# Kernel tuning notes

Measured on AMD Instinct MI355X. Metric: run time of the kernel, lower is better.

The kernel has to match this reference:

```python
import jax, jax.numpy as jnp
import numpy as np

BATCH, SEQ, DMODEL, DHID = 4, 4096, 1024, 1024
R_MIN, R_MAX = 0.9, 0.99
MAX_PHASE = np.pi / 50  # module overrides ctor arg with pi/50
EPS = 1e-5


def setup_inputs() -> dict:
    key = jax.random.key(0)
    ks = jax.random.split(key, 8)
    # nu_init
    u1 = jax.random.uniform(ks[0], (DHID,)) * (1 - EPS) + EPS
    mag_sq = u1 * (R_MAX ** 2 - R_MIN ** 2) + R_MIN ** 2
    nu_log = jnp.log(-0.5 * jnp.log(mag_sq + EPS))
    # theta_init
    u2 = jax.random.uniform(ks[1], (DHID,)) * (1 - EPS) + EPS
    theta_log = jnp.log(MAX_PHASE * u2)
    B_re = jax.random.normal(ks[2], (DHID, DMODEL)) / np.sqrt(2 * DMODEL)
    B_im = jax.random.normal(ks[3], (DHID, DMODEL)) / np.sqrt(2 * DMODEL)
    C_re = jax.random.normal(ks[4], (DMODEL, DHID)) / np.sqrt(DHID)
    C_im = jax.random.normal(ks[5], (DMODEL, DHID)) / np.sqrt(DHID)
    D_skip = jax.random.normal(ks[6], (DMODEL,))
    inputs = jax.random.normal(ks[7], (BATCH, SEQ, DMODEL), dtype=jnp.float32)
    return {"inputs": inputs, "nu_log": nu_log, "theta_log": theta_log,
            "B_re": B_re, "B_im": B_im, "C_re": C_re, "C_im": C_im,
            "D_skip": D_skip}


def reference(inputs, nu_log, theta_log, B_re, B_im, C_re, C_im, D_skip):
    nu = jnp.exp(nu_log)
    theta = jnp.exp(theta_log)
    diag_lambda = jnp.exp(-nu + 1j * theta)            # [H] complex
    # forward recomputes gamma_log from nu_log (parameter gamma_log unused)
    gamma_log = 0.5 * jnp.log(1 - jnp.exp(-2 * jnp.exp(nu_log)) + EPS)
    B_norm = (B_re + 1j * B_im) * jnp.exp(gamma_log)[:, None]  # [H, D]
    inputs_c = inputs.astype(jnp.complex64)
    Bu = jnp.einsum('hd,btd->bth', B_norm, inputs_c)   # [B, T, H]

    def step(h, bu_t):
        h = diag_lambda * h + bu_t
        return h, h

    h0 = jnp.zeros((inputs.shape[0], diag_lambda.shape[0]), dtype=Bu.dtype)
    _, hs = jax.lax.scan(step, h0, jnp.swapaxes(Bu, 0, 1))  # [T, B, H]
    hs = jnp.swapaxes(hs, 0, 1)                              # [B, T, H]
    C_complex = C_re + 1j * C_im                              # [D, H]
    out = jnp.einsum('bth,dh->btd', hs, C_complex).real + inputs * D_skip
    return out.astype(jnp.float32)
```

## Files before the change

kernel.cpp:

```cpp
#include <hip/hip_runtime.h>


typedef __bf16 bf16x8 __attribute__((ext_vector_type(8)));
typedef float floatx4 __attribute__((ext_vector_type(4)));

__device__ __forceinline__ unsigned short f2bf(float f) {
  unsigned u = __float_as_uint(f);
  u += 0x7fffu + ((u >> 16) & 1u);
  return (unsigned short)(u >> 16);
}
__device__ __forceinline__ float bf2f(unsigned short s) {
  return __uint_as_float(((unsigned)s) << 16);
}


__global__ void prep_params(const float* __restrict__ nu_log,
                            const float* __restrict__ theta_log,
                            float* __restrict__ lam,
                            float* __restrict__ lamL,
                            float* __restrict__ gamma)
{
  int h = blockIdx.x * 256 + threadIdx.x;
  float nu = expf(nu_log[h]);
  float th = expf(theta_log[h]);
  float r = expf(-nu);
  lam[h]        = r * cosf(th);
  lam[1024 + h] = r * sinf(th);
  float rL = expf(-128.0f * nu);
  lamL[h]        = rL * cosf(128.0f * th);
  lamL[1024 + h] = rL * sinf(128.0f * th);
  gamma[h] = sqrtf(1.0f - expf(-2.0f * nu) + 1e-5f);
}

__global__ void prep_B(const float* __restrict__ B_re, const float* __restrict__ B_im,
                       const float* __restrict__ gamma, unsigned short* __restrict__ Bcat)
{
  int tid = blockIdx.x * 256 + threadIdx.x;
  int n = tid >> 10;
  int d = tid & 1023;
  int h = n & 1023;
  float v = (n < 1024 ? B_re[h * 1024 + d] : B_im[h * 1024 + d]) * gamma[h];
  Bcat[tid] = f2bf(v);
}

__global__ void prep_C(const float* __restrict__ C_re, const float* __restrict__ C_im,
                       unsigned short* __restrict__ Ccat)
{
  int tid = blockIdx.x * 256 + threadIdx.x;
  int d = tid >> 11;
  int k = tid & 2047;
  float v = (k < 1024) ? C_re[d * 1024 + k] : -C_im[d * 1024 + (k - 1024)];
  Ccat[tid] = f2bf(v);
}

__global__ void conv_inputs(const float* __restrict__ in, unsigned short* __restrict__ outb)
{
  int tid = blockIdx.x * 256 + threadIdx.x;
  float4 v = ((const float4*)in)[tid];
  unsigned lo = (unsigned)f2bf(v.x) | ((unsigned)f2bf(v.y) << 16);
  unsigned hi = (unsigned)f2bf(v.z) | ((unsigned)f2bf(v.w) << 16);
  ((uint2*)outb)[tid] = make_uint2(lo, hi);
}


#define GLDS(gp, lp) __builtin_amdgcn_global_load_lds(                        \
      (const __attribute__((address_space(1))) void*)(gp),                    \
      (__attribute__((address_space(3))) void*)(lp), 16, 0, 0)

#define STAGE(kt, buf) do {                                                   \
    const int _ko = (kt) * 32;                                                \
    GLDS(gA0 + _ko, &As[(buf)][lofs0]);                                       \
    GLDS(gA1 + _ko, &As[(buf)][lofs1]);                                       \
    GLDS(gB0 + _ko, &Bs[(buf)][lofs0]);                                       \
    GLDS(gB1 + _ko, &Bs[(buf)][lofs1]);                                       \
  } while (0)

#define BODY(buf) do {                                                        \
    bf16x8 af[8], bf[4];                                                      \
    _Pragma("unroll")                                                         \
    for (int i = 0; i < 8; ++i) {                                             \
      const int r = wm * 128 + i * 16 + lm;                                   \
      af[i] = *reinterpret_cast<const bf16x8*>(                               \
          &As[(buf)][r * 32 + (q ^ ((r >> 1) & 3)) * 8]);                     \
    }                                                                         \
    _Pragma("unroll")                                                         \
    for (int j = 0; j < 4; ++j) {                                             \
      const int r = wn * 64 + j * 16 + lm;                                    \
      bf[j] = *reinterpret_cast<const bf16x8*>(                               \
          &Bs[(buf)][r * 32 + (q ^ ((r >> 1) & 3)) * 8]);                     \
    }                                                                         \
    __builtin_amdgcn_s_setprio(1);                                            \
    _Pragma("unroll")                                                         \
    for (int i = 0; i < 8; ++i)                                               \
      _Pragma("unroll")                                                       \
      for (int j = 0; j < 4; ++j)                                             \
        acc[i][j] = __builtin_amdgcn_mfma_f32_16x16x32_bf16(                  \
            af[i], bf[j], acc[i][j], 0, 0, 0);                                \
    __builtin_amdgcn_s_setprio(0);                                            \
  } while (0)

#define RING_SYNC(vm) do {                                                    \
    __builtin_amdgcn_sched_barrier(0);                                        \
    asm volatile("s_waitcnt vmcnt(" #vm ")" ::: "memory");                    \
    __builtin_amdgcn_s_barrier();                                             \
    asm volatile("" ::: "memory");                                            \
  } while (0)

template <int EPI>
__global__ __launch_bounds__(512, 2) void gemm256_kernel(
    const unsigned short* __restrict__ A,
    const unsigned short* __restrict__ Bt,
    void* __restrict__ Cout,
    int M, int N, int K,
    const float* __restrict__ skip_in,
    const float* __restrict__ skip_w)
{
  __shared__ __align__(16) unsigned short As[4][256 * 32];
  __shared__ __align__(16) unsigned short Bs[4][256 * 32];

  const int tid  = threadIdx.x;
  const int lane = tid & 63;
  const int wave = tid >> 6;
  const int wm = wave >> 2;
  const int wn = wave & 3;

  const int flat    = blockIdx.x;
  const int xcd     = flat & 7;
  const int local   = flat >> 3;
  const int m_tile  = xcd * 8 + (local & 7);
  const int n_tile  = local >> 3;
  const int m0 = m_tile * 256;
  const int n0 = n_tile * 256;

  const int ldr = lane >> 2;
  const int pos = lane & 3;
  const int lm  = lane & 15;
  const int q   = lane >> 4;

  const int r0 = wave * 32 + ldr;
  const int r1 = r0 + 16;
  const int ca0 = pos ^ ((r0 >> 1) & 3);
  const int ca1 = pos ^ ((r1 >> 1) & 3);

  const unsigned short* gA0 = A  + (size_t)(m0 + r0) * K + ca0 * 8;
  const unsigned short* gA1 = A  + (size_t)(m0 + r1) * K + ca1 * 8;
  const unsigned short* gB0 = Bt + (size_t)(n0 + r0) * K + ca0 * 8;
  const unsigned short* gB1 = Bt + (size_t)(n0 + r1) * K + ca1 * 8;
  const int lofs0 = r0 * 32 + pos * 8;
  const int lofs1 = r1 * 32 + pos * 8;

  floatx4 acc[8][4];
#pragma unroll
  for (int i = 0; i < 8; ++i)
#pragma unroll
    for (int j = 0; j < 4; ++j)
      acc[i][j] = (floatx4){0.f, 0.f, 0.f, 0.f};

  const int KT = K >> 5;

  STAGE(0, 0);
  STAGE(1, 1);
  STAGE(2, 2);
  asm volatile("s_waitcnt vmcnt(8)" ::: "memory");
  __builtin_amdgcn_s_barrier();
  asm volatile("" ::: "memory");

  for (int kt = 0; kt + 3 < KT; ++kt) {
    STAGE(kt + 3, (kt + 3) & 3);
    BODY(kt & 3);
    RING_SYNC(8);
  }
  BODY((KT - 3) & 3);
  RING_SYNC(4);
  BODY((KT - 2) & 3);
  RING_SYNC(0);
  BODY((KT - 1) & 3);

#pragma unroll
  for (int i = 0; i < 8; ++i) {
#pragma unroll
    for (int j = 0; j < 4; ++j) {
      const int row0 = m0 + wm * 128 + i * 16 + q * 4;
      const int col  = n0 + wn * 64 + j * 16 + lm;
#pragma unroll
      for (int r = 0; r < 4; ++r) {
        const size_t idx = (size_t)(row0 + r) * N + col;
        if (EPI == 0) {
          ((unsigned short*)Cout)[idx] = f2bf(acc[i][j][r]);
        } else {
          ((float*)Cout)[idx] = acc[i][j][r] + skip_in[idx] * skip_w[col];
        }
      }
    }
  }
}


__global__ void scan_finals(const unsigned short* __restrict__ Bu,
                            const float* __restrict__ lam,
                            float2* __restrict__ finals)
{
  int tid = blockIdx.x * 256 + threadIdx.x;
  int h = tid & 1023, c = (tid >> 10) & 31, b = tid >> 15;
  float lre = lam[h], lim = lam[1024 + h];
  const unsigned short* p = Bu + ((size_t)(b * 4096 + c * 128) * 2048) + h;
  float yre = 0.f, yim = 0.f;
#pragma unroll 4
  for (int t = 0; t < 128; ++t) {
    float ure = bf2f(p[0]);
    float uim = bf2f(p[1024]);
    float nre = fmaf(lre, yre, fmaf(-lim, yim, ure));
    float nim = fmaf(lre, yim, fmaf(lim, yre, uim));
    yre = nre; yim = nim;
    p += 2048;
  }
  finals[tid] = make_float2(yre, yim);
}

__global__ void scan_carries(const float2* __restrict__ finals,
                             const float* __restrict__ lamL,
                             float2* __restrict__ carry)
{
  int tid = blockIdx.x * 256 + threadIdx.x;
  int h = tid & 1023, b = tid >> 10;
  float Lre = lamL[h], Lim = lamL[1024 + h];
  float Hre = 0.f, Him = 0.f;
  for (int c = 0; c < 32; ++c) {
    size_t i = ((size_t)(b * 32 + c) << 10) + h;
    carry[i] = make_float2(Hre, Him);
    float2 f = finals[i];
    float nre = fmaf(Lre, Hre, fmaf(-Lim, Him, f.x));
    float nim = fmaf(Lre, Him, fmaf(Lim, Hre, f.y));
    Hre = nre; Him = nim;
  }
}

__global__ void scan_apply(const float* __restrict__ lam,
                           const float2* __restrict__ carry,
                           unsigned short* __restrict__ Bu)
{
  int tid = blockIdx.x * 256 + threadIdx.x;
  int h = tid & 1023, c = (tid >> 10) & 31, b = tid >> 15;
  float lre = lam[h], lim = lam[1024 + h];
  float2 cv = carry[tid];
  float yre = cv.x, yim = cv.y;
  unsigned short* p = Bu + ((size_t)(b * 4096 + c * 128) * 2048) + h;
#pragma unroll 4
  for (int t = 0; t < 128; ++t) {
    float ure = bf2f(p[0]);
    float uim = bf2f(p[1024]);
    float nre = fmaf(lre, yre, fmaf(-lim, yim, ure));
    float nim = fmaf(lre, yim, fmaf(lim, yre, uim));
    yre = nre; yim = nim;
    p[0]    = f2bf(yre);
    p[1024] = f2bf(yim);
    p += 2048;
  }
}


extern "C" void kernel_launch(void* const* d_in, const int* in_sizes, int n_in,
                              void* d_out, int out_size, void* d_ws, size_t ws_size,
                              hipStream_t stream)
{
  const float* inputs    = (const float*)d_in[0];
  const float* nu_log    = (const float*)d_in[1];
  const float* theta_log = (const float*)d_in[2];
  const float* B_re      = (const float*)d_in[3];
  const float* B_im      = (const float*)d_in[4];
  const float* C_re      = (const float*)d_in[5];
  const float* C_im      = (const float*)d_in[6];
  const float* D_skip    = (const float*)d_in[7];
  float* out = (float*)d_out;

  char* ws = (char*)d_ws;
  float* lam   = (float*)ws;
  float* lamL  = lam + 2048;
  float* gamma = lamL + 2048;
  unsigned short* inp_bf = (unsigned short*)(ws + (1 << 16));
  unsigned short* Bcat   = inp_bf + (size_t)16384 * 1024;
  unsigned short* Ccat   = Bcat   + (size_t)2048 * 1024;
  unsigned short* Bu     = Ccat   + (size_t)1024 * 2048;
  float2* finals = (float2*)(Bu + (size_t)16384 * 2048);
  float2* carry  = finals + 131072;

  prep_params<<<4,    256, 0, stream>>>(nu_log, theta_log, lam, lamL, gamma);
  prep_B     <<<8192, 256, 0, stream>>>(B_re, B_im, gamma, Bcat);
  prep_C     <<<8192, 256, 0, stream>>>(C_re, C_im, Ccat);
  conv_inputs<<<16384,256, 0, stream>>>(inputs, inp_bf);

  gemm256_kernel<0><<<512, 512, 0, stream>>>(
      inp_bf, Bcat, Bu, 16384, 2048, 1024, nullptr, nullptr);

  scan_finals <<<512, 256, 0, stream>>>(Bu, lam, finals);
  scan_carries<<<16,  256, 0, stream>>>(finals, lamL, carry);
  scan_apply  <<<512, 256, 0, stream>>>(lam, carry, Bu);

  gemm256_kernel<1><<<256, 512, 0, stream>>>(
      Bu, Ccat, out, 16384, 1024, 2048, inputs, D_skip);
}
```

Baseline: 363.0 us.

## Split GEMM k-step into two barrier-separated phases interleaving LDS reads, loads, MFMAs

Each k-iteration of the 256x256 bf16 GEMM now runs as two half-phases. Each phase reads half of the A fragments from LDS, issues half of the next tile's global-to-LDS loads, and does 16 MFMAs between workgroup barriers, in a ping-pong style. The aim is to overlap LDS reads and global loads with matrix math across the waves and to cut register pressure by holding only 4 A fragments at a time. In exchange it doubles the number of barriers per k-step, and the hand-placed vmcnt waits and sched barriers depend on exact ordering.

```diff
diff --git a/kernel.cpp b/kernel.cpp
--- a/kernel.cpp
+++ b/kernel.cpp
@@ -75,35 +75,41 @@
     GLDS(gB1 + _ko, &Bs[(buf)][lofs1]);                                       \
   } while (0)
 
-#define BODY(buf) do {                                                        \
-    bf16x8 af[8], bf[4];                                                      \
-    _Pragma("unroll")                                                         \
-    for (int i = 0; i < 8; ++i) {                                             \
-      const int r = wm * 128 + i * 16 + lm;                                   \
-      af[i] = *reinterpret_cast<const bf16x8*>(                               \
-          &As[(buf)][r * 32 + (q ^ ((r >> 1) & 3)) * 8]);                     \
-    }                                                                         \
+#define READ_B(buf) do {                                                      \
     _Pragma("unroll")                                                         \
     for (int j = 0; j < 4; ++j) {                                             \
       const int r = wn * 64 + j * 16 + lm;                                    \
-      bf[j] = *reinterpret_cast<const bf16x8*>(                               \
+      bfr[j] = *reinterpret_cast<const bf16x8*>(                              \
           &Bs[(buf)][r * 32 + (q ^ ((r >> 1) & 3)) * 8]);                     \
     }                                                                         \
+  } while (0)
+
+#define READ_A(buf, i0) do {                                                  \
+    _Pragma("unroll")                                                         \
+    for (int i = 0; i < 4; ++i) {                                             \
+      const int r = wm * 128 + ((i0) + i) * 16 + lm;                          \
+      afr[i] = *reinterpret_cast<const bf16x8*>(                              \
+          &As[(buf)][r * 32 + (q ^ ((r >> 1) & 3)) * 8]);                     \
+    }                                                                         \
+  } while (0)
+
+#define MFMA16(i0) do {                                                       \
     __builtin_amdgcn_s_setprio(1);                                            \
     _Pragma("unroll")                                                         \
-    for (int i = 0; i < 8; ++i)                                               \
+    for (int i = 0; i < 4; ++i)                                               \
       _Pragma("unroll")                                                       \
       for (int j = 0; j < 4; ++j)                                             \
-        acc[i][j] = __builtin_amdgcn_mfma_f32_16x16x32_bf16(                  \
-            af[i], bf[j], acc[i][j], 0, 0, 0);                                \
+        acc[(i0) + i][j] = __builtin_amdgcn_mfma_f32_16x16x32_bf16(           \
+            afr[i], bfr[j], acc[(i0) + i][j], 0, 0, 0);                       \
     __builtin_amdgcn_s_setprio(0);                                            \
   } while (0)
 
-#define RING_SYNC(vm) do {                                                    \
+#define BAR() do {                                                            \
     __builtin_amdgcn_sched_barrier(0);                                        \
-    asm volatile("s_waitcnt vmcnt(" #vm ")" ::: "memory");                    \
+    asm volatile("" ::: "memory");                                            \
     __builtin_amdgcn_s_barrier();                                             \
     asm volatile("" ::: "memory");                                            \
+    __builtin_amdgcn_sched_barrier(0);                                        \
   } while (0)
 
 template <int EPI>
@@ -166,15 +172,65 @@
   asm volatile("" ::: "memory");
 
   for (int kt = 0; kt + 3 < KT; ++kt) {
-    STAGE(kt + 3, (kt + 3) & 3);
-    BODY(kt & 3);
-    RING_SYNC(8);
-  }
-  BODY((KT - 3) & 3);
-  RING_SYNC(4);
-  BODY((KT - 2) & 3);
-  RING_SYNC(0);
-  BODY((KT - 1) & 3);
+    const int cur = kt & 3;
+    const int b3  = (kt + 3) & 3;
+    const int ko3 = (kt + 3) * 32;
+    bf16x8 afr[4], bfr[4];
+
+    READ_B(cur);
+    READ_A(cur, 0);
+    GLDS(gA0 + ko3, &As[b3][lofs0]);
+    GLDS(gA1 + ko3, &As[b3][lofs1]);
+    BAR();
+    MFMA16(0);
+    BAR();
+
+    READ_A(cur, 4);
+    GLDS(gB0 + ko3, &Bs[b3][lofs0]);
+    GLDS(gB1 + ko3, &Bs[b3][lofs1]);
+    asm volatile("s_waitcnt vmcnt(8)" ::: "memory");
+    BAR();
+    MFMA16(4);
+    BAR();
+  }
+
+  {
+    const int cur = (KT - 3) & 3;
+    bf16x8 afr[4], bfr[4];
+    READ_B(cur);
+    READ_A(cur, 0);
+    BAR();
+    MFMA16(0);
+    BAR();
+    READ_A(cur, 4);
+    asm volatile("s_waitcnt vmcnt(4)" ::: "memory");
+    BAR();
+    MFMA16(4);
+    BAR();
+  }
+  {
+    const int cur = (KT - 2) & 3;
+    bf16x8 afr[4], bfr[4];
+    READ_B(cur);
+    READ_A(cur, 0);
+    BAR();
+    MFMA16(0);
+    BAR();
+    READ_A(cur, 4);
+    asm volatile("s_waitcnt vmcnt(0)" ::: "memory");
+    BAR();
+    MFMA16(4);
+    BAR();
+  }
+  {
+    const int cur = (KT - 1) & 3;
+    bf16x8 afr[4], bfr[4];
+    READ_B(cur);
+    READ_A(cur, 0);
+    MFMA16(0);
+    READ_A(cur, 4);
+    MFMA16(4);
+  }
 
 #pragma unroll
   for (int i = 0; i < 8; ++i) {
```

Result: faster. 330.1 us (-9.1%).

## Split GEMM k-step into two half-phases interleaving LDS reads, global loads, MFMAs

Applied to the files above, without the earlier changes.

Restructures the GEMM main loop into two phases per k-tile. Each phase issues half of the LDS fragment reads plus one operand's global-to-LDS prefetch, then runs 16 MFMAs, with explicit sched_barriers, lgkmcnt waits and workgroup barriers in between. The aim is to overlap LDS reads and global loads with matrix work, in a ping-pong style schedule. It adds an extra barrier per k-tile, which may cost more sync overhead than the overlap saves.

```diff
diff --git a/kernel.cpp b/kernel.cpp
--- a/kernel.cpp
+++ b/kernel.cpp
@@ -75,35 +75,98 @@
     GLDS(gB1 + _ko, &Bs[(buf)][lofs1]);                                       \
   } while (0)
 
-#define BODY(buf) do {                                                        \
-    bf16x8 af[8], bf[4];                                                      \
-    _Pragma("unroll")                                                         \
-    for (int i = 0; i < 8; ++i) {                                             \
-      const int r = wm * 128 + i * 16 + lm;                                   \
-      af[i] = *reinterpret_cast<const bf16x8*>(                               \
-          &As[(buf)][r * 32 + (q ^ ((r >> 1) & 3)) * 8]);                     \
-    }                                                                         \
+#define GLDS_A(kt) do {                                                       \
+    const int _ko = (kt) * 32;  const int _b = (kt) & 3;                      \
+    GLDS(gA0 + _ko, &As[_b][lofs0]);                                          \
+    GLDS(gA1 + _ko, &As[_b][lofs1]);                                          \
+  } while (0)
+
+#define GLDS_B(kt) do {                                                       \
+    const int _ko = (kt) * 32;  const int _b = (kt) & 3;                      \
+    GLDS(gB0 + _ko, &Bs[_b][lofs0]);                                          \
+    GLDS(gB1 + _ko, &Bs[_b][lofs1]);                                          \
+  } while (0)
+
+#define RD_B(buf) do {                                                        \
     _Pragma("unroll")                                                         \
     for (int j = 0; j < 4; ++j) {                                             \
       const int r = wn * 64 + j * 16 + lm;                                    \
-      bf[j] = *reinterpret_cast<const bf16x8*>(                               \
+      bfr[j] = *reinterpret_cast<const bf16x8*>(                              \
           &Bs[(buf)][r * 32 + (q ^ ((r >> 1) & 3)) * 8]);                     \
     }                                                                         \
+  } while (0)
+
+#define RD_A(buf, i0) do {                                                    \
+    _Pragma("unroll")                                                         \
+    for (int i = 0; i < 4; ++i) {                                             \
+      const int r = wm * 128 + ((i0) + i) * 16 + lm;                          \
+      afr[(i0) + i] = *reinterpret_cast<const bf16x8*>(                       \
+          &As[(buf)][r * 32 + (q ^ ((r >> 1) & 3)) * 8]);                     \
+    }                                                                         \
+  } while (0)
+
+#define MFMA16(i0) do {                                                       \
     __builtin_amdgcn_s_setprio(1);                                            \
     _Pragma("unroll")                                                         \
-    for (int i = 0; i < 8; ++i)                                               \
+    for (int i = 0; i < 4; ++i)                                               \
       _Pragma("unroll")                                                       \
       for (int j = 0; j < 4; ++j)                                             \
-        acc[i][j] = __builtin_amdgcn_mfma_f32_16x16x32_bf16(                  \
-            af[i], bf[j], acc[i][j], 0, 0, 0);                                \
+        acc[(i0) + i][j] = __builtin_amdgcn_mfma_f32_16x16x32_bf16(           \
+            afr[(i0) + i], bfr[j], acc[(i0) + i][j], 0, 0, 0);                \
     __builtin_amdgcn_s_setprio(0);                                            \
   } while (0)
 
-#define RING_SYNC(vm) do {                                                    \
-    __builtin_amdgcn_sched_barrier(0);                                        \
-    asm volatile("s_waitcnt vmcnt(" #vm ")" ::: "memory");                    \
+#define SB0() __builtin_amdgcn_sched_barrier(0)
+
+#define VMW(n) do {                                                           \
+    SB0();                                                                    \
+    asm volatile("s_waitcnt vmcnt(" #n ")" ::: "memory");                     \
+    SB0();                                                                    \
+  } while (0)
+
+#define BAR() do {                                                            \
+    SB0();                                                                    \
+    asm volatile("" ::: "memory");                                            \
     __builtin_amdgcn_s_barrier();                                             \
     asm volatile("" ::: "memory");                                            \
+    SB0();                                                                    \
+  } while (0)
+
+#define LGKM0() do {                                                          \
+    asm volatile("s_waitcnt lgkmcnt(0)" ::: "memory");                        \
+    SB0();                                                                    \
+  } while (0)
+
+#define BODY(kt_) do {                                                        \
+    const int _cur = (kt_) & 3;                                               \
+                                                                 \
+    RD_B(_cur);                                                               \
+    RD_A(_cur, 0);                                                            \
+    GLDS_A((kt_) + 3);                                                        \
+    BAR();                                                                    \
+    LGKM0();                                                                  \
+    MFMA16(0);                                                                \
+                                                                 \
+    RD_A(_cur, 4);                                                            \
+    GLDS_B((kt_) + 3);                                                        \
+    VMW(8);                                                                   \
+    BAR();                                                                    \
+    LGKM0();                                                                  \
+    MFMA16(4);                                                                \
+  } while (0)
+
+#define TAIL(kt_, vm_) do {                                                   \
+    const int _cur = (kt_) & 3;                                               \
+    RD_B(_cur);                                                               \
+    RD_A(_cur, 0);                                                            \
+    BAR();                                                                    \
+    LGKM0();                                                                  \
+    MFMA16(0);                                                                \
+    RD_A(_cur, 4);                                                            \
+    VMW(vm_);                                                                 \
+    BAR();                                                                    \
+    LGKM0();                                                                  \
+    MFMA16(4);                                                                \
   } while (0)
 
 template <int EPI>
@@ -158,23 +221,29 @@
 
   const int KT = K >> 5;
 
+  bf16x8 afr[8], bfr[4];
+
   STAGE(0, 0);
   STAGE(1, 1);
   STAGE(2, 2);
-  asm volatile("s_waitcnt vmcnt(8)" ::: "memory");
-  __builtin_amdgcn_s_barrier();
-  asm volatile("" ::: "memory");
-
-  for (int kt = 0; kt + 3 < KT; ++kt) {
-    STAGE(kt + 3, (kt + 3) & 3);
-    BODY(kt & 3);
-    RING_SYNC(8);
-  }
-  BODY((KT - 3) & 3);
-  RING_SYNC(4);
-  BODY((KT - 2) & 3);
-  RING_SYNC(0);
-  BODY((KT - 1) & 3);
+  VMW(8);
+  BAR();
+
+  for (int kt = 0; kt + 3 < KT; ++kt)
+    BODY(kt);
+
+  TAIL(KT - 3, 4);
+  TAIL(KT - 2, 0);
+  {
+    const int _cur = (KT - 1) & 3;
+    RD_B(_cur);
+    RD_A(_cur, 0);
+    LGKM0();
+    MFMA16(0);
+    RD_A(_cur, 4);
+    LGKM0();
+    MFMA16(4);
+  }
 
 #pragma unroll
   for (int i = 0; i < 8; ++i) {
```

After: 327.7 us. 9.7% less time.
